# Optimization experiments

Measured on AMD Instinct MI355X. Metric: run time of the kernel, lower is better.

Reference implementation:

```python
import jax, jax.numpy as jnp
import numpy as np

B, DIM, H, W = 8, 256, 128, 128
P = 4               # patch_size
HEADS = 8
HD = DIM // HEADS   # head dim = 32
CPB_HIDDEN = 512    # hidden width of the dynamic RPE MLP


def setup_inputs() -> dict:
    key = jax.random.key(0)
    ks = jax.random.split(key, 12)
    s = 0.02
    return {
        "x": jax.random.normal(ks[0], (B, DIM, H, W), dtype=jnp.float32),
        # PatchEmbed2d: Conv2d(dim, dim, kernel=P, stride=P)  weight [O, I, P, P]
        "w_embed": jax.random.normal(ks[1], (DIM, DIM, P, P), dtype=jnp.float32) * s,
        "b_embed": jnp.zeros((DIM,), dtype=jnp.float32),
        # DynamicPosEncoder: MLP(2 -> CPB_HIDDEN -> HEADS) on relative coords
        "cpb_w1": jax.random.normal(ks[2], (CPB_HIDDEN, 2), dtype=jnp.float32) * s,
        "cpb_b1": jnp.zeros((CPB_HIDDEN,), dtype=jnp.float32),
        "cpb_w2": jax.random.normal(ks[3], (HEADS, CPB_HIDDEN), dtype=jnp.float32) * s,
        # MaskAttention2d
        "w_qkv": jax.random.normal(ks[4], (3 * DIM, DIM), dtype=jnp.float32) * s,
        "b_qkv": jnp.zeros((3 * DIM,), dtype=jnp.float32),
        "w_proj": jax.random.normal(ks[5], (DIM, DIM), dtype=jnp.float32) * s,
        "b_proj": jnp.zeros((DIM,), dtype=jnp.float32),
        # PatchUnEmbed2d: ConvTranspose2d(dim, dim, kernel=P, stride=P)  weight [I, O, P, P]
        "w_unembed": jax.random.normal(ks[6], (DIM, DIM, P, P), dtype=jnp.float32) * s,
        "b_unembed": jnp.zeros((DIM,), dtype=jnp.float32),
    }


def _rpe_bias(Hp, Wp, cpb_w1, cpb_b1, cpb_w2):
    """Dynamic relative position bias -> [HEADS, N, N], N = Hp*Wp."""
    # continuous relative-coordinate table [(2Hp-1)*(2Wp-1), 2], normalized to [-1, 1]
    rh = (jnp.arange(2 * Hp - 1, dtype=jnp.float32) - (Hp - 1)) / max(Hp - 1, 1)
    rw = (jnp.arange(2 * Wp - 1, dtype=jnp.float32) - (Wp - 1)) / max(Wp - 1, 1)
    rel = jnp.stack(jnp.meshgrid(rh, rw, indexing="ij"), axis=-1).reshape(-1, 2)
    table = jax.nn.relu(rel @ cpb_w1.T + cpb_b1) @ cpb_w2.T  # [(2Hp-1)(2Wp-1), HEADS]
    # static relative position index [N, N]
    ch = np.arange(Hp)
    cw = np.arange(Wp)
    coords = np.stack(np.meshgrid(ch, cw, indexing="ij")).reshape(2, -1)  # [2, N]
    d = coords[:, :, None] - coords[:, None, :]                           # [2, N, N]
    idx = (d[0] + Hp - 1) * (2 * Wp - 1) + (d[1] + Wp - 1)               # [N, N]
    bias = table[jnp.asarray(idx)]                                        # [N, N, HEADS]
    return bias.transpose(2, 0, 1)                                        # [HEADS, N, N]


def reference(x, w_embed, b_embed, cpb_w1, cpb_b1, cpb_w2,
              w_qkv, b_qkv, w_proj, b_proj, w_unembed, b_unembed):
    Bx, C, Hf, Wf = x.shape
    Hp, Wp = Hf // P, Wf // P
    N = Hp * Wp
    # ---- patch embed: Conv2d(k=P, s=P) as block reshape + einsum ----
    xr = x.reshape(Bx, C, Hp, P, Wp, P)
    z = jnp.einsum("bchpwq,ocpq->bohw", xr, w_embed) + b_embed[None, :, None, None]
    # ---- dynamic RPE bias ----
    bias = _rpe_bias(Hp, Wp, cpb_w1, cpb_b1, cpb_w2)  # [HEADS, N, N]
    # ---- multi-head self-attention over the Hp*Wp grid ----
    tok = z.reshape(Bx, C, N).transpose(0, 2, 1)                     # [B, N, C]
    qkv = tok @ w_qkv.T + b_qkv                                       # [B, N, 3C]
    qkv = qkv.reshape(Bx, N, 3, HEADS, HD).transpose(2, 0, 3, 1, 4)   # [3, B, H, N, hd]
    q, k, v = qkv[0], qkv[1], qkv[2]
    scale = HD ** -0.5
    attn = jnp.einsum("bhnd,bhmd->bhnm", q * scale, k) + bias[None]   # [B, H, N, N]
    attn = jax.nn.softmax(attn, axis=-1)
    out = jnp.einsum("bhnm,bhmd->bhnd", attn, v)                      # [B, H, N, hd]
    out = out.transpose(0, 2, 1, 3).reshape(Bx, N, C)
    out = out @ w_proj.T + b_proj                                     # [B, N, C]
    z2 = out.transpose(0, 2, 1).reshape(Bx, C, Hp, Wp)
    # ---- patch unembed: ConvTranspose2d(k=P, s=P) as einsum + block reshape ----
    y = jnp.einsum("bchw,copq->bohpwq", z2, w_unembed)
    y = y.reshape(Bx, C, Hf, Wf) + b_unembed[None, :, None, None]
    return y
```

## Files before the change

kernel.cpp:

```cpp
#include <hip/hip_runtime.h>
#include <cstdint>
#include <cstddef>


typedef __bf16 bf16x8 __attribute__((ext_vector_type(8)));
typedef float f32x4 __attribute__((ext_vector_type(4)));
typedef unsigned short u16x4 __attribute__((ext_vector_type(4)));

__device__ __forceinline__ unsigned short f2bf(float f) {
  unsigned u = __builtin_bit_cast(unsigned, f);
  u += 0x7fffu + ((u >> 16) & 1u);
  return (unsigned short)(u >> 16);
}
__device__ __forceinline__ float bf2f(unsigned short u) {
  return __builtin_bit_cast(float, ((unsigned)u) << 16);
}

__device__ __forceinline__ void async_ld16(const void* g, void* l) {
  __builtin_amdgcn_global_load_lds(
      (const __attribute__((address_space(1))) void*)g,
      (__attribute__((address_space(3))) void*)l, 16, 0, 0);
}

__global__ __launch_bounds__(256) void rpe_table_kernel(
    const float* __restrict__ w1, const float* __restrict__ b1,
    const float* __restrict__ w2, float* __restrict__ tableT) {
  int t = blockIdx.x * 256 + threadIdx.x;
  if (t >= 3969) return;
  int a = t / 63, c = t - a * 63;
  float rh = (float)(a - 31) * (1.0f / 31.0f);
  float rw = (float)(c - 31) * (1.0f / 31.0f);
  float acc[8];
#pragma unroll
  for (int h = 0; h < 8; h++) acc[h] = 0.f;
  for (int j = 0; j < 512; j++) {
    float hv = fmaxf(rh * w1[2 * j] + rw * w1[2 * j + 1] + b1[j], 0.f);
#pragma unroll
    for (int h = 0; h < 8; h++) acc[h] += hv * w2[h * 512 + j];
  }
#pragma unroll
  for (int h = 0; h < 8; h++) tableT[h * 4096 + t] = acc[h];
}

__global__ __launch_bounds__(256) void cvt_bf16_kernel(
    const float* __restrict__ src, unsigned short* __restrict__ dst, int n8) {
  int i = blockIdx.x * 256 + threadIdx.x;
  if (i >= n8) return;
  const float4* s4 = (const float4*)src + (size_t)i * 2;
  float4 a = s4[0], b = s4[1];
  unsigned short t[8] = {f2bf(a.x), f2bf(a.y), f2bf(a.z), f2bf(a.w),
                         f2bf(b.x), f2bf(b.y), f2bf(b.z), f2bf(b.w)};
  *(uint4*)(dst + (size_t)i * 8) = *(const uint4*)t;
}

__global__ __launch_bounds__(256) void transpose_cvt_kernel(
    const float* __restrict__ src, unsigned short* __restrict__ dst) {
  __shared__ float tile[32][33];
  int bx = blockIdx.x;
  int by = blockIdx.y;
  int tx = threadIdx.x & 31, ty = threadIdx.x >> 5;
#pragma unroll
  for (int r = 0; r < 32; r += 8)
    tile[ty + r][tx] = src[(size_t)(by * 32 + ty + r) * 4096 + bx * 32 + tx];
  __syncthreads();
#pragma unroll
  for (int r = 0; r < 32; r += 8)
    dst[(size_t)(bx * 32 + ty + r) * 256 + by * 32 + tx] = f2bf(tile[tx][ty + r]);
}

__global__ __launch_bounds__(256) void im2col_bf16_kernel(
    const float* __restrict__ x, unsigned short* __restrict__ A) {
  int gid = blockIdx.x * 256 + threadIdx.x;
  int bn = gid & 8191;
  int c = gid >> 13;
  int b = bn >> 10;
  int hw = bn & 1023;
  int h = hw >> 5, w = hw & 31;
  const float4* x4 = (const float4*)x;
  int base = ((b * 256 + c) * 128 + 4 * h) * 32 + w;
  unsigned short t[16];
#pragma unroll
  for (int p = 0; p < 4; p++) {
    float4 v = x4[base + p * 32];
    t[p * 4 + 0] = f2bf(v.x); t[p * 4 + 1] = f2bf(v.y);
    t[p * 4 + 2] = f2bf(v.z); t[p * 4 + 3] = f2bf(v.w);
  }
  unsigned short* dst = A + (size_t)bn * 4096 + c * 16;
  *(uint4*)dst = *(const uint4*)t;
  *(uint4*)(dst + 8) = *(const uint4*)(t + 8);
}

__global__ __launch_bounds__(256) void splitk_reduce_kernel(
    const float* __restrict__ part, const float* __restrict__ bias,
    unsigned short* __restrict__ out) {
  size_t i = ((size_t)blockIdx.x * 256 + threadIdx.x) * 8;
  const float4* p = (const float4*)(part + i);
  const size_t s4 = 2097152 / 4;
  float4 a0 = p[0], a1 = p[1];
#pragma unroll
  for (int s = 1; s < 4; s++) {
    float4 b0 = p[s * s4], b1 = p[s * s4 + 1];
    a0.x += b0.x; a0.y += b0.y; a0.z += b0.z; a0.w += b0.w;
    a1.x += b1.x; a1.y += b1.y; a1.z += b1.z; a1.w += b1.w;
  }
  int col = (int)(i & 255);
  unsigned short t8[8] = {
      f2bf(a0.x + bias[col + 0]), f2bf(a0.y + bias[col + 1]),
      f2bf(a0.z + bias[col + 2]), f2bf(a0.w + bias[col + 3]),
      f2bf(a1.x + bias[col + 4]), f2bf(a1.y + bias[col + 5]),
      f2bf(a1.z + bias[col + 6]), f2bf(a1.w + bias[col + 7])};
  *(uint4*)(out + i) = *(const uint4*)t8;
}

template <int CMODE>
__global__ __launch_bounds__(256) void gemm_mfma_kernel(
    const unsigned short* __restrict__ A, const unsigned short* __restrict__ B,
    const float* __restrict__ bias, void* __restrict__ Cv,
    int M, int N, int K, int lda, int ldb, int ldc) {
  __shared__ unsigned short As[2 * 128 * 32];
  __shared__ unsigned short Bs[2 * 128 * 32];
  int tid = threadIdx.x;
  int lane = tid & 63;
  int wave = tid >> 6;
  int m0 = blockIdx.y * 128, n0 = blockIdx.x * 128;
  int wm = (wave & 1) * 64, wn = (wave >> 1) * 64;

  if (CMODE == 4) {
    int s = blockIdx.z;
    A += (size_t)s * K;
    B += (size_t)s * K;
    Cv = (void*)((float*)Cv + (size_t)s * M * N);
  }

  f32x4 acc[4][4];
#pragma unroll
  for (int i = 0; i < 4; i++)
#pragma unroll
    for (int j = 0; j < 4; j++) acc[i][j] = (f32x4){0.f, 0.f, 0.f, 0.f};

  int f0 = tid, f1 = tid + 256;
  const unsigned short* Ag0 = A + (size_t)(m0 + (f0 >> 2)) * lda + (f0 & 3) * 8;
  const unsigned short* Ag1 = A + (size_t)(m0 + (f1 >> 2)) * lda + (f1 & 3) * 8;
  const unsigned short* Bg0 = B + (size_t)(n0 + (f0 >> 2)) * ldb + (f0 & 3) * 8;
  const unsigned short* Bg1 = B + (size_t)(n0 + (f1 >> 2)) * ldb + (f1 & 3) * 8;
  unsigned short* Al0 = As + f0 * 8;
  unsigned short* Al1 = As + f1 * 8;
  unsigned short* Bl0 = Bs + f0 * 8;
  unsigned short* Bl1 = Bs + f1 * 8;

  int fr = lane & 15;
  int fh = lane >> 4;

  int ntiles = K >> 5;
  async_ld16(Ag0, Al0);
  async_ld16(Ag1, Al1);
  async_ld16(Bg0, Bl0);
  async_ld16(Bg1, Bl1);
  __syncthreads();

  for (int t = 0; t < ntiles; t++) {
    int cur = (t & 1) << 12;
    int nxt = cur ^ 4096;
    if (t + 1 < ntiles) {
      int kn = (t + 1) << 5;
      async_ld16(Ag0 + kn, Al0 + nxt);
      async_ld16(Ag1 + kn, Al1 + nxt);
      async_ld16(Bg0 + kn, Bl0 + nxt);
      async_ld16(Bg1 + kn, Bl1 + nxt);
    }
    const unsigned short* Asc = As + cur;
    const unsigned short* Bsc = Bs + cur;
    bf16x8 af[4], bfr[4];
#pragma unroll
    for (int tt = 0; tt < 4; tt++) {
      af[tt] = *(const bf16x8*)(Asc + (wm + tt * 16 + fr) * 32 + fh * 8);
      bfr[tt] = *(const bf16x8*)(Bsc + (wn + tt * 16 + fr) * 32 + fh * 8);
    }
#pragma unroll
    for (int mt = 0; mt < 4; mt++)
#pragma unroll
      for (int nt = 0; nt < 4; nt++)
        acc[mt][nt] = __builtin_amdgcn_mfma_f32_16x16x32_bf16(
            af[mt], bfr[nt], acc[mt][nt], 0, 0, 0);
    __syncthreads();
  }

#pragma unroll
  for (int mt = 0; mt < 4; mt++) {
    int row0 = m0 + wm + mt * 16 + fh * 4;
    if (CMODE == 2) {
      int b = row0 >> 10, hp = (row0 >> 5) & 31, wp = row0 & 31;
      size_t rowoff0 = (size_t)b * 4194304 + hp * 512 + wp * 4;
      float* y = (float*)Cv;
#pragma unroll
      for (int nt = 0; nt < 4; nt++) {
        int col = n0 + wn + nt * 16 + fr;
        int o = col >> 4, p = (col >> 2) & 3, q = col & 3;
        size_t coloff = (size_t)o * 16384 + p * 128 + q;
        float bv = bias[o];
#pragma unroll
        for (int r = 0; r < 4; r++)
          y[rowoff0 + r * 4 + coloff] = acc[mt][nt][r] + bv;
      }
    } else if (CMODE == 3) {
      unsigned short* base = (unsigned short*)Cv;
#pragma unroll
      for (int nt = 0; nt < 4; nt++) {
        int col = n0 + wn + nt * 16 + fr;
        int which = col >> 8, hh = (col >> 5) & 7, d = col & 31;
        float bv = bias[col];
#pragma unroll
        for (int r = 0; r < 4; r++) {
          int row = row0 + r;
          int bb = row >> 10, nn = row & 1023;
          int bh = bb * 8 + hh;
          float v = acc[mt][nt][r] + bv;
          if (which == 0) v *= 0.17677669529663687f;
          size_t addr;
          if (which < 2)
            addr = (size_t)which * 2097152 + ((size_t)bh * 1024 + nn) * 32 + d;
          else
            addr = (size_t)2 * 2097152 + (size_t)bh * 32768 + (size_t)d * 1024 + nn;
          base[addr] = f2bf(v);
        }
      }
    } else if (CMODE == 4) {
      float* Cp = (float*)Cv;
#pragma unroll
      for (int nt = 0; nt < 4; nt++) {
        int col = n0 + wn + nt * 16 + fr;
#pragma unroll
        for (int r = 0; r < 4; r++)
          Cp[(size_t)(row0 + r) * ldc + col] = acc[mt][nt][r];
      }
    } else {
#pragma unroll
      for (int nt = 0; nt < 4; nt++) {
        int col = n0 + wn + nt * 16 + fr;
        float bv = bias ? bias[col] : 0.f;
        unsigned short* C = (unsigned short*)Cv;
#pragma unroll
        for (int r = 0; r < 4; r++)
          C[(size_t)(row0 + r) * ldc + col] = f2bf(acc[mt][nt][r] + bv);
      }
    }
  }
}

__global__ __launch_bounds__(512) void attn_mfma_kernel(
    const unsigned short* __restrict__ Qb, const unsigned short* __restrict__ Kb,
    const unsigned short* __restrict__ Vtb,
    const float* __restrict__ tableT,
    unsigned short* __restrict__ out) {
  __shared__ float th[3972];
  __shared__ unsigned short Ps[2][8][1088];

  int tid = threadIdx.x;
  int lane = tid & 63, w = tid >> 6;
  int n = lane & 15, g = lane >> 4;
  int blk = blockIdx.x;
  int h = blk & 7, b = (blk >> 3) & 7, qt = blk >> 6;
  int bh = b * 8 + h;
  int q0 = qt * 128;

  const unsigned short* Qg = Qb + ((size_t)bh * 1024 + q0) * 32;
  const unsigned short* Kg = Kb + (size_t)bh * 1024 * 32;
  const unsigned short* Vg = Vtb + (size_t)bh * 32 * 1024;
  const float* tg = tableT + (size_t)h * 4096;

  for (int i = tid; i < 3969; i += 512) th[i] = tg[i];

  bf16x8 qf = *(const bf16x8*)(Qg + (size_t)(w * 16 + n) * 32 + g * 8);

  __syncthreads();

  f32x4 oacc[2];
  oacc[0] = (f32x4){0.f, 0.f, 0.f, 0.f};
  oacc[1] = (f32x4){0.f, 0.f, 0.f, 0.f};
  float m_run = -1e30f, l_run = 0.f;

  int q = q0 + w * 16 + n;
  int tbase = (q >> 5) * 63 + (q & 31);

  unsigned short* Pw0 = &Ps[0][w][0];
  unsigned short* Pw1 = &Ps[1][w][0];

  bf16x8 kf[2][4], vf[4];
#pragma unroll
  for (int mt = 0; mt < 4; mt++)
    kf[0][mt] = *(const bf16x8*)(Kg + (size_t)(mt * 16 + n) * 32 + g * 8);

#pragma unroll
  for (int t = 0; t < 16; t++) {
    const int cur = t & 1, nxt = cur ^ 1;
    const int k0 = t * 64;

#pragma unroll
    for (int i = 0; i < 4; i++)
      vf[i] = *(const bf16x8*)(Vg + (size_t)((i & 1) * 16 + n) * 1024 + k0 +
                               (i >> 1) * 32 + g * 8);
    if (t < 15) {
#pragma unroll
      for (int mt = 0; mt < 4; mt++)
        kf[nxt][mt] = *(const bf16x8*)(Kg + (size_t)(k0 + 64 + mt * 16 + n) * 32 +
                                       g * 8);
    }

    f32x4 s[4];
    __builtin_amdgcn_s_setprio(1);
#pragma unroll
    for (int mt = 0; mt < 4; mt++)
      s[mt] = __builtin_amdgcn_mfma_f32_16x16x32_bf16(
          kf[cur][mt], qf, (f32x4){0.f, 0.f, 0.f, 0.f}, 0, 0, 0);
    __builtin_amdgcn_s_setprio(0);

#pragma unroll
    for (int mt = 0; mt < 4; mt++) {
      int kb = k0 + mt * 16 + g * 4;
      int ib = tbase + (31 - (kb >> 5)) * 63 + (31 - (kb & 31));
      s[mt][0] += th[ib];
      s[mt][1] += th[ib - 1];
      s[mt][2] += th[ib - 2];
      s[mt][3] += th[ib - 3];
    }

    float mx = -1e30f;
#pragma unroll
    for (int mt = 0; mt < 4; mt++)
#pragma unroll
      for (int r = 0; r < 4; r++) mx = fmaxf(mx, s[mt][r]);
    mx = fmaxf(mx, __shfl_xor(mx, 16, 64));
    mx = fmaxf(mx, __shfl_xor(mx, 32, 64));
    float m_new = fmaxf(m_run, mx);
    float alpha = __expf(m_run - m_new);
    m_run = m_new;

    unsigned short* Pw = cur ? Pw1 : Pw0;
    float ls = 0.f;
#pragma unroll
    for (int mt = 0; mt < 4; mt++) {
#pragma unroll
      for (int r = 0; r < 4; r++) {
        float p = __expf(s[mt][r] - m_new);
        s[mt][r] = p;
        ls += p;
      }
      u16x4 pk = {f2bf(s[mt][0]), f2bf(s[mt][1]), f2bf(s[mt][2]),
                  f2bf(s[mt][3])};
      *(u16x4*)(Pw + n * 68 + mt * 16 + g * 4) = pk;
    }
    l_run = l_run * alpha + ls;

#pragma unroll
    for (int dt = 0; dt < 2; dt++)
#pragma unroll
      for (int r = 0; r < 4; r++) oacc[dt][r] *= alpha;
    __builtin_amdgcn_s_setprio(1);
#pragma unroll
    for (int kt = 0; kt < 2; kt++) {
      bf16x8 pf = *(const bf16x8*)(Pw + n * 68 + kt * 32 + g * 8);
      oacc[0] = __builtin_amdgcn_mfma_f32_16x16x32_bf16(vf[kt * 2 + 0], pf,
                                                        oacc[0], 0, 0, 0);
      oacc[1] = __builtin_amdgcn_mfma_f32_16x16x32_bf16(vf[kt * 2 + 1], pf,
                                                        oacc[1], 0, 0, 0);
    }
    __builtin_amdgcn_s_setprio(0);
  }

  float l = l_run;
  l += __shfl_xor(l, 16, 64);
  l += __shfl_xor(l, 32, 64);
  float invl = 1.f / l;
  unsigned short* ob = out + ((size_t)(b * 1024 + q) * 256) + h * 32;
#pragma unroll
  for (int dt = 0; dt < 2; dt++) {
    u16x4 o4 = {f2bf(oacc[dt][0] * invl), f2bf(oacc[dt][1] * invl),
                f2bf(oacc[dt][2] * invl), f2bf(oacc[dt][3] * invl)};
    *(u16x4*)(ob + dt * 16 + g * 4) = o4;
  }
}

extern "C" void kernel_launch(void* const* d_in, const int* in_sizes, int n_in,
                              void* d_out, int out_size, void* d_ws, size_t ws_size,
                              hipStream_t stream) {
  const float* x         = (const float*)d_in[0];
  const float* w_embed   = (const float*)d_in[1];
  const float* b_embed   = (const float*)d_in[2];
  const float* cpb_w1    = (const float*)d_in[3];
  const float* cpb_b1    = (const float*)d_in[4];
  const float* cpb_w2    = (const float*)d_in[5];
  const float* w_qkv     = (const float*)d_in[6];
  const float* b_qkv     = (const float*)d_in[7];
  const float* w_proj    = (const float*)d_in[8];
  const float* b_proj    = (const float*)d_in[9];
  const float* w_unembed = (const float*)d_in[10];
  const float* b_unembed = (const float*)d_in[11];
  float* out = (float*)d_out;

  char* w = (char*)d_ws;
  unsigned short* Abig  = (unsigned short*)w; w += (size_t)8192 * 4096 * 2;
  unsigned short* tok   = (unsigned short*)w; w += (size_t)8192 * 256 * 2;
  unsigned short* wE    = (unsigned short*)w; w += (size_t)1048576 * 2;
  unsigned short* wQ    = (unsigned short*)w; w += (size_t)196608 * 2;
  unsigned short* wP    = (unsigned short*)w; w += (size_t)65536 * 2;
  unsigned short* wUt   = (unsigned short*)w; w += (size_t)1048576 * 2;
  float*          tableT= (float*)w;          w += (size_t)32768 * 4;
  float*          PART  = (float*)w;          w += (size_t)8388608 * 4;

  unsigned short* qkvB  = (unsigned short*)PART;
  unsigned short* attno = (unsigned short*)((char*)PART + 12582912);
  unsigned short* z2    = (unsigned short*)((char*)PART + 16777216);
  unsigned short* Qb  = qkvB;
  unsigned short* Kb  = qkvB + 2097152;
  unsigned short* Vtb = qkvB + 2 * 2097152;

  cvt_bf16_kernel<<<512, 256, 0, stream>>>(w_embed, wE, 131072);
  cvt_bf16_kernel<<<96, 256, 0, stream>>>(w_qkv, wQ, 24576);
  cvt_bf16_kernel<<<32, 256, 0, stream>>>(w_proj, wP, 8192);
  transpose_cvt_kernel<<<dim3(128, 8), 256, 0, stream>>>(w_unembed, wUt);
  im2col_bf16_kernel<<<8192, 256, 0, stream>>>(x, Abig);
  rpe_table_kernel<<<16, 256, 0, stream>>>(cpb_w1, cpb_b1, cpb_w2, tableT);

  gemm_mfma_kernel<4><<<dim3(2, 64, 4), 256, 0, stream>>>(
      Abig, wE, nullptr, PART, 8192, 256, 1024, 4096, 4096, 256);
  splitk_reduce_kernel<<<1024, 256, 0, stream>>>(PART, b_embed, tok);

  gemm_mfma_kernel<3><<<dim3(6, 64), 256, 0, stream>>>(
      tok, wQ, b_qkv, qkvB, 8192, 768, 256, 256, 256, 0);

  attn_mfma_kernel<<<512, 512, 0, stream>>>(Qb, Kb, Vtb, tableT, attno);

  gemm_mfma_kernel<4><<<dim3(2, 64, 4), 256, 0, stream>>>(
      attno, wP, nullptr, (float*)Abig, 8192, 256, 64, 256, 256, 256);
  splitk_reduce_kernel<<<1024, 256, 0, stream>>>((float*)Abig, b_proj, z2);

  gemm_mfma_kernel<2><<<dim3(32, 64), 256, 0, stream>>>(
      z2, wUt, b_unembed, out, 8192, 4096, 256, 256, 256, 0);
}
```

Baseline: 547.4 us.

## Fuse im2col into patch-embed GEMM and restructure attention K prefetch

Removes the separate im2col kernel that wrote a 64 MB bf16 matrix. A new embed GEMM reads fp32 x directly, converts it to bf16 in registers and stores it into LDS, with register double-buffering and an XCD-aware block remap. The attention loop is restructured into two half-steps per iteration with separate K register buffers and a simplified bias index. This saves a large round trip to global memory, at the cost of strided fp32 loads inside the GEMM.

```diff
diff --git a/kernel.cpp b/kernel.cpp
--- a/kernel.cpp
+++ b/kernel.cpp
@@ -20,6 +20,13 @@
   __builtin_amdgcn_global_load_lds(
       (const __attribute__((address_space(1))) void*)g,
       (__attribute__((address_space(3))) void*)l, 16, 0, 0);
+}
+
+__device__ __forceinline__ void cvt8_store(unsigned short* dst, float4 a,
+                                           float4 b) {
+  unsigned short t[8] = {f2bf(a.x), f2bf(a.y), f2bf(a.z), f2bf(a.w),
+                         f2bf(b.x), f2bf(b.y), f2bf(b.z), f2bf(b.w)};
+  *(uint4*)dst = *(const uint4*)t;
 }
 
 __global__ __launch_bounds__(256) void rpe_table_kernel(
@@ -68,28 +75,6 @@
     dst[(size_t)(bx * 32 + ty + r) * 256 + by * 32 + tx] = f2bf(tile[tx][ty + r]);
 }
 
-__global__ __launch_bounds__(256) void im2col_bf16_kernel(
-    const float* __restrict__ x, unsigned short* __restrict__ A) {
-  int gid = blockIdx.x * 256 + threadIdx.x;
-  int bn = gid & 8191;
-  int c = gid >> 13;
-  int b = bn >> 10;
-  int hw = bn & 1023;
-  int h = hw >> 5, w = hw & 31;
-  const float4* x4 = (const float4*)x;
-  int base = ((b * 256 + c) * 128 + 4 * h) * 32 + w;
-  unsigned short t[16];
-#pragma unroll
-  for (int p = 0; p < 4; p++) {
-    float4 v = x4[base + p * 32];
-    t[p * 4 + 0] = f2bf(v.x); t[p * 4 + 1] = f2bf(v.y);
-    t[p * 4 + 2] = f2bf(v.z); t[p * 4 + 3] = f2bf(v.w);
-  }
-  unsigned short* dst = A + (size_t)bn * 4096 + c * 16;
-  *(uint4*)dst = *(const uint4*)t;
-  *(uint4*)(dst + 8) = *(const uint4*)(t + 8);
-}
-
 __global__ __launch_bounds__(256) void splitk_reduce_kernel(
     const float* __restrict__ part, const float* __restrict__ bias,
     unsigned short* __restrict__ out) {
@@ -110,6 +95,103 @@
       f2bf(a1.x + bias[col + 4]), f2bf(a1.y + bias[col + 5]),
       f2bf(a1.z + bias[col + 6]), f2bf(a1.w + bias[col + 7])};
   *(uint4*)(out + i) = *(const uint4*)t8;
+}
+
+__global__ __launch_bounds__(256) void gemm_embed_kernel(
+    const float* __restrict__ x, const unsigned short* __restrict__ B,
+    float* __restrict__ Cpart) {
+  __shared__ unsigned short As[2 * 128 * 32];
+  __shared__ unsigned short Bs[2 * 128 * 32];
+  int tid = threadIdx.x;
+  int lane = tid & 63, wave = tid >> 6;
+
+  int L = blockIdx.x;
+  int xcd = L & 7, j = L >> 3;
+  int pair = xcd * 32 + (j >> 1);
+  int n0 = (j & 1) * 128;
+  int z = pair & 3, y = pair >> 2;
+  int m0 = y * 128;
+  int wm = (wave & 1) * 64, wn = (wave >> 1) * 64;
+  int fr = lane & 15, fh = lane >> 4;
+
+  f32x4 acc[4][4];
+#pragma unroll
+  for (int i = 0; i < 4; i++)
+#pragma unroll
+    for (int jj = 0; jj < 4; jj++) acc[i][jj] = (f32x4){0.f, 0.f, 0.f, 0.f};
+
+  int f0 = tid, f1 = tid + 256;
+  const unsigned short* Bg0 =
+      B + (size_t)(n0 + (f0 >> 2)) * 4096 + z * 1024 + (f0 & 3) * 8;
+  const unsigned short* Bg1 =
+      B + (size_t)(n0 + (f1 >> 2)) * 4096 + z * 1024 + (f1 & 3) * 8;
+  unsigned short* Bl0 = Bs + f0 * 8;
+  unsigned short* Bl1 = Bs + f1 * 8;
+
+  const float4* x4 = (const float4*)x;
+  int r0 = f0 >> 2, ch0 = f0 & 3;
+  int m_0 = m0 + r0, b_0 = m_0 >> 10, hp0 = (m_0 >> 5) & 31, wp0 = m_0 & 31;
+  int k_0 = z * 1024 + ch0 * 8, c_0 = k_0 >> 4, p_0 = (k_0 >> 2) & 3;
+  const float4* xp0 =
+      x4 + (size_t)((b_0 * 256 + c_0) * 128 + hp0 * 4 + p_0) * 32 + wp0;
+  int r1 = f1 >> 2, ch1 = f1 & 3;
+  int m_1 = m0 + r1, b_1 = m_1 >> 10, hp1 = (m_1 >> 5) & 31, wp1 = m_1 & 31;
+  int k_1 = z * 1024 + ch1 * 8, c_1 = k_1 >> 4, p_1 = (k_1 >> 2) & 3;
+  const float4* xp1 =
+      x4 + (size_t)((b_1 * 256 + c_1) * 128 + hp1 * 4 + p_1) * 32 + wp1;
+  unsigned short* Al0 = As + f0 * 8;
+  unsigned short* Al1 = As + f1 * 8;
+
+  float4 a00 = xp0[0], a01 = xp0[32], a10 = xp1[0], a11 = xp1[32];
+  xp0 += 8192; xp1 += 8192;
+  async_ld16(Bg0, Bl0);
+  async_ld16(Bg1, Bl1);
+  cvt8_store(Al0, a00, a01);
+  cvt8_store(Al1, a10, a11);
+  __syncthreads();
+
+  for (int t = 0; t < 32; t++) {
+    int cur = (t & 1) << 12, nxt = cur ^ 4096;
+    if (t < 31) {
+      a00 = xp0[0]; a01 = xp0[32]; a10 = xp1[0]; a11 = xp1[32];
+      xp0 += 8192; xp1 += 8192;
+      int kn = (t + 1) << 5;
+      async_ld16(Bg0 + kn, Bl0 + nxt);
+      async_ld16(Bg1 + kn, Bl1 + nxt);
+    }
+    const unsigned short* Asc = As + cur;
+    const unsigned short* Bsc = Bs + cur;
+    bf16x8 af[4], bfr[4];
+#pragma unroll
+    for (int tt = 0; tt < 4; tt++) {
+      af[tt] = *(const bf16x8*)(Asc + (wm + tt * 16 + fr) * 32 + fh * 8);
+      bfr[tt] = *(const bf16x8*)(Bsc + (wn + tt * 16 + fr) * 32 + fh * 8);
+    }
+#pragma unroll
+    for (int mt = 0; mt < 4; mt++)
+#pragma unroll
+      for (int nt = 0; nt < 4; nt++)
+        acc[mt][nt] = __builtin_amdgcn_mfma_f32_16x16x32_bf16(
+            af[mt], bfr[nt], acc[mt][nt], 0, 0, 0);
+    if (t < 31) {
+      cvt8_store(Al0 + nxt, a00, a01);
+      cvt8_store(Al1 + nxt, a10, a11);
+    }
+    __syncthreads();
+  }
+
+  float* Cp = Cpart + (size_t)z * 2097152;
+#pragma unroll
+  for (int mt = 0; mt < 4; mt++) {
+    int row0 = m0 + wm + mt * 16 + fh * 4;
+#pragma unroll
+    for (int nt = 0; nt < 4; nt++) {
+      int col = n0 + wn + nt * 16 + fr;
+#pragma unroll
+      for (int r = 0; r < 4; r++)
+        Cp[(size_t)(row0 + r) * 256 + col] = acc[mt][nt][r];
+    }
+  }
 }
 
 template <int CMODE>
@@ -269,9 +351,7 @@
   const float* tg = tableT + (size_t)h * 4096;
 
   for (int i = tid; i < 3969; i += 512) th[i] = tg[i];
-
   bf16x8 qf = *(const bf16x8*)(Qg + (size_t)(w * 16 + n) * 32 + g * 8);
-
   __syncthreads();
 
   f32x4 oacc[2];
@@ -280,44 +360,35 @@
   float m_run = -1e30f, l_run = 0.f;
 
   int q = q0 + w * 16 + n;
-  int tbase = (q >> 5) * 63 + (q & 31);
-
-  unsigned short* Pw0 = &Ps[0][w][0];
-  unsigned short* Pw1 = &Ps[1][w][0];
-
-  bf16x8 kf[2][4], vf[4];
+  int tbase = (q >> 5) * 63 + (q & 31) + 1984;
+
+  unsigned short* PwA = &Ps[0][w][0];
+  unsigned short* PwB = &Ps[1][w][0];
+
+  bf16x8 kfA[4], kfB[4];
 #pragma unroll
   for (int mt = 0; mt < 4; mt++)
-    kf[0][mt] = *(const bf16x8*)(Kg + (size_t)(mt * 16 + n) * 32 + g * 8);
-
-#pragma unroll
-  for (int t = 0; t < 16; t++) {
-    const int cur = t & 1, nxt = cur ^ 1;
-    const int k0 = t * 64;
-
+    kfA[mt] = *(const bf16x8*)(Kg + (size_t)(mt * 16 + n) * 32 + g * 8);
+
+  auto half_step = [&](const bf16x8 (&kf)[4], int k0, unsigned short* Pw) {
+    bf16x8 vf[4];
 #pragma unroll
     for (int i = 0; i < 4; i++)
       vf[i] = *(const bf16x8*)(Vg + (size_t)((i & 1) * 16 + n) * 1024 + k0 +
                                (i >> 1) * 32 + g * 8);
-    if (t < 15) {
-#pragma unroll
-      for (int mt = 0; mt < 4; mt++)
-        kf[nxt][mt] = *(const bf16x8*)(Kg + (size_t)(k0 + 64 + mt * 16 + n) * 32 +
-                                       g * 8);
-    }
 
     f32x4 s[4];
     __builtin_amdgcn_s_setprio(1);
 #pragma unroll
     for (int mt = 0; mt < 4; mt++)
       s[mt] = __builtin_amdgcn_mfma_f32_16x16x32_bf16(
-          kf[cur][mt], qf, (f32x4){0.f, 0.f, 0.f, 0.f}, 0, 0, 0);
+          kf[mt], qf, (f32x4){0.f, 0.f, 0.f, 0.f}, 0, 0, 0);
     __builtin_amdgcn_s_setprio(0);
 
 #pragma unroll
     for (int mt = 0; mt < 4; mt++) {
       int kb = k0 + mt * 16 + g * 4;
-      int ib = tbase + (31 - (kb >> 5)) * 63 + (31 - (kb & 31));
+      int ib = tbase - (kb >> 5) * 63 - (kb & 31);
       s[mt][0] += th[ib];
       s[mt][1] += th[ib - 1];
       s[mt][2] += th[ib - 2];
@@ -335,7 +406,6 @@
     float alpha = __expf(m_run - m_new);
     m_run = m_new;
 
-    unsigned short* Pw = cur ? Pw1 : Pw0;
     float ls = 0.f;
 #pragma unroll
     for (int mt = 0; mt < 4; mt++) {
@@ -365,6 +435,22 @@
                                                         oacc[1], 0, 0, 0);
     }
     __builtin_amdgcn_s_setprio(0);
+  };
+
+  for (int tt = 0; tt < 8; tt++) {
+    int k0 = tt * 128;
+#pragma unroll
+    for (int mt = 0; mt < 4; mt++)
+      kfB[mt] = *(const bf16x8*)(Kg + (size_t)(k0 + 64 + mt * 16 + n) * 32 +
+                                 g * 8);
+    half_step(kfA, k0, PwA);
+    if (tt < 7) {
+#pragma unroll
+      for (int mt = 0; mt < 4; mt++)
+        kfA[mt] = *(const bf16x8*)(Kg + (size_t)(k0 + 128 + mt * 16 + n) * 32 +
+                                   g * 8);
+    }
+    half_step(kfB, k0 + 64, PwB);
   }
 
   float l = l_run;
@@ -398,7 +484,7 @@
   float* out = (float*)d_out;
 
   char* w = (char*)d_ws;
-  unsigned short* Abig  = (unsigned short*)w; w += (size_t)8192 * 4096 * 2;
+  float*          ProjP = (float*)w;          w += (size_t)8388608 * 4;
   unsigned short* tok   = (unsigned short*)w; w += (size_t)8192 * 256 * 2;
   unsigned short* wE    = (unsigned short*)w; w += (size_t)1048576 * 2;
   unsigned short* wQ    = (unsigned short*)w; w += (size_t)196608 * 2;
@@ -418,11 +504,9 @@
   cvt_bf16_kernel<<<96, 256, 0, stream>>>(w_qkv, wQ, 24576);
   cvt_bf16_kernel<<<32, 256, 0, stream>>>(w_proj, wP, 8192);
   transpose_cvt_kernel<<<dim3(128, 8), 256, 0, stream>>>(w_unembed, wUt);
-  im2col_bf16_kernel<<<8192, 256, 0, stream>>>(x, Abig);
   rpe_table_kernel<<<16, 256, 0, stream>>>(cpb_w1, cpb_b1, cpb_w2, tableT);
 
-  gemm_mfma_kernel<4><<<dim3(2, 64, 4), 256, 0, stream>>>(
-      Abig, wE, nullptr, PART, 8192, 256, 1024, 4096, 4096, 256);
+  gemm_embed_kernel<<<512, 256, 0, stream>>>(x, wE, PART);
   splitk_reduce_kernel<<<1024, 256, 0, stream>>>(PART, b_embed, tok);
 
   gemm_mfma_kernel<3><<<dim3(6, 64), 256, 0, stream>>>(
@@ -431,8 +515,8 @@
   attn_mfma_kernel<<<512, 512, 0, stream>>>(Qb, Kb, Vtb, tableT, attno);
 
   gemm_mfma_kernel<4><<<dim3(2, 64, 4), 256, 0, stream>>>(
-      attno, wP, nullptr, (float*)Abig, 8192, 256, 64, 256, 256, 256);
-  splitk_reduce_kernel<<<1024, 256, 0, stream>>>((float*)Abig, b_proj, z2);
+      attno, wP, nullptr, ProjP, 8192, 256, 64, 256, 256, 256);
+  splitk_reduce_kernel<<<1024, 256, 0, stream>>>(ProjP, b_proj, z2);
 
   gemm_mfma_kernel<2><<<dim3(32, 64), 256, 0, stream>>>(
       z2, wUt, b_unembed, out, 8192, 4096, 256, 256, 256, 0);
```

After: 496.1 us. 9.4% less time.
